# Kernel tuning notes

Hardware: AMD Instinct MI355X
Metric: run time of the kernel (lower is better)

The kernel has to match this reference:

```python
import jax, jax.numpy as jnp
import numpy as np

B, S, D_MODEL = 2, 2048, 4096
N_HEADS, N_KV, HEAD_DIM = 32, 8, 128
N_GROUPS = N_HEADS // N_KV
QKV_DIM = (N_HEADS + 2 * N_KV) * HEAD_DIM


def _rope_tables(seq_len, head_dim, base=10000.0):
    inv_freq = 1.0 / (base ** (np.arange(0, head_dim, 2, dtype=np.float32) / head_dim))
    t = np.arange(seq_len, dtype=np.float32)
    freqs = np.outer(t, inv_freq)                      # [S, D/2]
    emb = np.concatenate([freqs, freqs], axis=-1)      # [S, D]
    return jnp.asarray(np.cos(emb)), jnp.asarray(np.sin(emb))


def setup_inputs() -> dict:
    key = jax.random.key(0)
    k1, k2, k3 = jax.random.split(key, 3)
    cos, sin = _rope_tables(S, HEAD_DIM)
    return {
        "hidden_states": jax.random.normal(k1, (B, S, D_MODEL), dtype=jnp.float32),
        "cos": cos,
        "sin": sin,
        "W_qkv": jax.random.normal(k2, (D_MODEL, QKV_DIM), dtype=jnp.float32) * (D_MODEL ** -0.5),
        "W_out": jax.random.normal(k3, (D_MODEL, D_MODEL), dtype=jnp.float32) * (D_MODEL ** -0.5),
    }


def _rotate_half(x):
    x1, x2 = jnp.split(x, 2, axis=-1)
    return jnp.concatenate([-x2, x1], axis=-1)


def _apply_rope(x, cos, sin):
    # x: [b, h, s, d]; cos/sin: [s, d]
    c = cos[None, None, :, :]
    s = sin[None, None, :, :]
    return x * c + _rotate_half(x) * s


def reference(hidden_states, cos, sin, W_qkv, W_out):
    b, s, _ = hidden_states.shape
    qkv = jnp.einsum("bsm,mq->bsq", hidden_states, W_qkv)
    q_end = N_HEADS * HEAD_DIM
    kv_sz = N_KV * HEAD_DIM
    q = qkv[..., :q_end].reshape(b, s, N_HEADS, HEAD_DIM).transpose(0, 2, 1, 3)
    k = qkv[..., q_end:q_end + kv_sz].reshape(b, s, N_KV, HEAD_DIM).transpose(0, 2, 1, 3)
    v = qkv[..., q_end + kv_sz:].reshape(b, s, N_KV, HEAD_DIM).transpose(0, 2, 1, 3)

    q = _apply_rope(q, cos, sin)          # [b, H, s, d]
    k = _apply_rope(k, cos, sin)          # [b, KV, s, d] (equiv. to repeat->rope->stride slice)

    # GQA without materializing repeated KV: group query heads per KV head.
    qg = q.reshape(b, N_KV, N_GROUPS, s, HEAD_DIM)
    scale = HEAD_DIM ** -0.5
    scores = jnp.einsum("bkgqd,bkpd->bkgqp", qg, k) * scale  # [b, KV, G, s, s]
    causal = jnp.tril(jnp.ones((s, s), dtype=bool))
    scores = jnp.where(causal, scores, jnp.finfo(scores.dtype).min)
    probs = jax.nn.softmax(scores, axis=-1)
    out = jnp.einsum("bkgqp,bkpd->bkgqd", probs, v)           # [b, KV, G, s, d]
    out = out.reshape(b, N_HEADS, s, HEAD_DIM).transpose(0, 2, 1, 3).reshape(b, s, D_MODEL)
    return jnp.einsum("bsm,mn->bsn", out, W_out)
```

## Files before the change

### kernel.cpp

```cpp
#include <hip/hip_runtime.h>


typedef __bf16 bf16;
typedef bf16 bf16x8 __attribute__((ext_vector_type(8)));
typedef bf16 bf16x4 __attribute__((ext_vector_type(4)));
typedef float f32x4 __attribute__((ext_vector_type(4)));
typedef unsigned int u32;
typedef u32 u32x4 __attribute__((ext_vector_type(4)));

#define B_ 2
#define S_ 2048
#define DM 4096
#define NH 32
#define NKV 8
#define HD 128
#define QKV_DIM 6144

typedef __attribute__((address_space(3))) void lds_void;
typedef const __attribute__((address_space(1))) void glb_void;

__device__ __forceinline__ void gld_lds16(const bf16* g, bf16* l) {
  __builtin_amdgcn_global_load_lds((glb_void*)g, (lds_void*)l, 16, 0, 0);
}

__device__ __forceinline__ u32 bf16bits(float x) {
  union { bf16 h; unsigned short s; } u;
  u.h = (bf16)x;
  return (u32)u.s;
}

__global__ __launch_bounds__(256) void cast_f32_bf16(const float* __restrict__ src,
                                                     bf16* __restrict__ dst, int n) {
  int i = (blockIdx.x * 256 + threadIdx.x) * 4;
  float4 v = *(const float4*)(src + i);
  bf16x4 o;
  o[0] = (bf16)v.x; o[1] = (bf16)v.y; o[2] = (bf16)v.z; o[3] = (bf16)v.w;
  *(bf16x4*)(dst + i) = o;
}

__global__ __launch_bounds__(256) void transpose_cast_w(const float* __restrict__ W,
                                                        bf16* __restrict__ Wt,
                                                        int K, int N) {
  __shared__ float tile[64][65];
  const int n0 = blockIdx.x * 64, k0 = blockIdx.y * 64;
  const int t = threadIdx.x, j = t & 63, i0 = t >> 6;
  for (int p = 0; p < 16; ++p) {
    int i = i0 + p * 4;
    tile[i][j] = W[(size_t)(k0 + i) * N + n0 + j];
  }
  __syncthreads();
  for (int p = 0; p < 16; ++p) {
    int n = i0 + p * 4;
    Wt[(size_t)(n0 + n) * K + k0 + j] = (bf16)tile[j][n];
  }
}

__global__ __launch_bounds__(256) void transpose_v(const bf16* __restrict__ qkv,
                                                   bf16* __restrict__ v_t) {
  __shared__ bf16 tile[64][65];
  const int s0 = blockIdx.x * 64;
  const int d0 = blockIdx.y * 64;
  const int bk = blockIdx.z;
  const int b = bk >> 3, kv = bk & 7;
  const int t = threadIdx.x, j = t & 63, i0 = t >> 6;
  const bf16* src = qkv + (size_t)b * S_ * QKV_DIM + 5120 + kv * HD;
  for (int p = 0; p < 16; ++p) {
    int i = i0 + p * 4;
    tile[i][j] = src[(size_t)(s0 + i) * QKV_DIM + d0 + j];
  }
  __syncthreads();
  bf16* dst = v_t + ((size_t)bk * HD + d0) * S_ + s0;
  for (int p = 0; p < 16; ++p) {
    int dd = i0 + p * 4;
    dst[(size_t)dd * S_ + j] = tile[j][dd];
  }
}

__global__ __launch_bounds__(128) void rope_kernel(const bf16* __restrict__ qkv,
                                                   const float* __restrict__ cosT,
                                                   const float* __restrict__ sinT,
                                                   bf16* __restrict__ q_r,
                                                   bf16* __restrict__ k_r) {
  const int bs = blockIdx.x;
  const int b = bs >> 11, s = bs & 2047;
  const int d = threadIdx.x;
  const float cv = cosT[s * HD + d];
  const float sv = sinT[s * HD + d];
  const bf16* row = qkv + (size_t)bs * QKV_DIM;
  const float scale = 0.08838834764831845f;
  for (int h = 0; h < NH; ++h) {
    float x = (float)row[h * HD + d];
    float xr = (d < 64) ? -(float)row[h * HD + d + 64] : (float)row[h * HD + d - 64];
    q_r[(((size_t)(b * NH + h)) * S_ + s) * HD + d] = (bf16)((x * cv + xr * sv) * scale);
  }
  for (int kv = 0; kv < NKV; ++kv) {
    float x = (float)row[DM + kv * HD + d];
    float xr = (d < 64) ? -(float)row[DM + kv * HD + d + 64] : (float)row[DM + kv * HD + d - 64];
    k_r[(((size_t)(b * NKV + kv)) * S_ + s) * HD + d] = (bf16)(x * cv + xr * sv);
  }
}

#define BAR() __builtin_amdgcn_s_barrier()
#define LGKM0() asm volatile("s_waitcnt lgkmcnt(0)" ::: "memory")
#define VM6() asm volatile("s_waitcnt vmcnt(6)" ::: "memory")
#define VM0() asm volatile("s_waitcnt vmcnt(0)" ::: "memory")
#define VMNONE() do {} while (0)
#define PRIO1() __builtin_amdgcn_s_setprio(1)
#define PRIO0() __builtin_amdgcn_s_setprio(0)

#define MFMA16(MH)                                                                   \
  do {                                                                               \
    _Pragma("unroll") for (int mm = 0; mm < 4; ++mm) {                               \
      _Pragma("unroll") for (int nn = 0; nn < 4; ++nn) {                             \
        acc[(MH)*4 + mm][nn] = __builtin_amdgcn_mfma_f32_16x16x32_bf16(              \
            af[mm], bfr[nn], acc[(MH)*4 + mm][nn], 0, 0, 0);                         \
      }                                                                              \
    }                                                                                \
  } while (0)

#define TILE4(T, P, VMEND)                                                           \
  do {                                                                               \
    ldA(P, 0, 0); ldB(P, 0);                                                         \
    stage_idx(4 * (T) + 7);                                                          \
    BAR(); LGKM0();                                                                  \
    PRIO1(); MFMA16(0); PRIO0(); BAR();                                              \
    ldA(P, 0, 1);                                                                    \
    stage_idx(4 * (T) + 8);                                                          \
    BAR(); LGKM0();                                                                  \
    PRIO1(); MFMA16(1); PRIO0(); BAR();                                              \
    ldA(P, 1, 0); ldB(P, 1);                                                         \
    stage_idx(4 * (T) + 9);                                                          \
    BAR(); LGKM0();                                                                  \
    PRIO1(); MFMA16(0); PRIO0(); BAR();                                              \
    ldA(P, 1, 1);                                                                    \
    stage_idx(4 * (T) + 10);                                                         \
    BAR(); LGKM0();                                                                  \
    PRIO1(); MFMA16(1); PRIO0();                                                     \
    VMEND; BAR();                                                                    \
  } while (0)

template <bool OUT_BF16>
__global__ __launch_bounds__(512, 2) void gemm256_bt(const bf16* __restrict__ A,
                                                     const bf16* __restrict__ Bt,
                                                     void* __restrict__ Cout,
                                                     int M, int N, int K) {
  extern __shared__ char lds[];
  const int NT = K >> 6;

  const int nwg = gridDim.x;
  const int cpx = nwg >> 3;
  const int wg = (blockIdx.x & 7) * cpx + (blockIdx.x >> 3);
  const int nbx = N >> 8;
  const int bx = wg % nbx, by = wg / nbx;
  const int m0 = by * 256, n0 = bx * 256;

  const int t = threadIdx.x;
  const int w = t >> 6, lane = t & 63;
  const int wr = w >> 2, wc = w & 3;
  const int quad = lane >> 4, c = lane & 15;

  const int aOff = (((wr * 128 + c) * 64 + quad * 16) ^ ((c & 8) << 2));
  const int bOff = (((wc * 64 + c) * 64 + quad * 16) ^ ((c & 8) << 2)) + 32768;

  const int srow = w * 32 + (lane >> 2);
  const int scol = (((lane & 3) ^ ((lane >> 4) & 2)) << 3);
  const bf16* Abase = A + (size_t)(m0 + srow) * K + scol;
  const bf16* Bbase = Bt + (size_t)(n0 + srow) * K + scol;
  const size_t rs16 = (size_t)16 * K;

  auto stage_idx = [&](int H) {
    if (H >= 4 * NT) return;
    const int tS = H >> 2, jS = H & 3;
    const int kh = jS >> 1;
    const int kbase = tS * 64 + kh * 32;
    const int regionOff = ((tS & 1) << 16) + ((jS & 1) << 15) + (kh << 14) + (w << 11);
    const bf16* g = ((jS & 1) ? Bbase : Abase) + kbase;
    char* l = lds + regionOff;
    gld_lds16(g, (bf16*)l);
    gld_lds16(g + rs16, (bf16*)(l + 1024));
  };

  bf16x8 af[4], bfr[4];
  auto ldA = [&](int P, int s, int mh) {
    const char* base = lds + P * 65536 + s * 16384 + mh * 4096 + aOff;
    af[0] = *(const bf16x8*)(base);
    af[1] = *(const bf16x8*)(base + 1024);
    af[2] = *(const bf16x8*)(base + 2048);
    af[3] = *(const bf16x8*)(base + 3072);
  };
  auto ldB = [&](int P, int s) {
    const char* base = lds + P * 65536 + s * 16384 + bOff;
    bfr[0] = *(const bf16x8*)(base);
    bfr[1] = *(const bf16x8*)(base + 1024);
    bfr[2] = *(const bf16x8*)(base + 2048);
    bfr[3] = *(const bf16x8*)(base + 3072);
  };

  f32x4 acc[8][4];
#pragma unroll
  for (int i = 0; i < 8; ++i)
#pragma unroll
    for (int j = 0; j < 4; ++j) acc[i][j] = (f32x4){0.f, 0.f, 0.f, 0.f};

#pragma unroll
  for (int hh = 0; hh < 7; ++hh) stage_idx(hh);
  VM6();
  BAR();

  for (int tt = 0; tt < NT - 2; tt += 2) {
    TILE4(tt, 0, VM6());
    TILE4(tt + 1, 1, VM6());
  }
  TILE4(NT - 2, 0, VM0());
  TILE4(NT - 1, 1, VMNONE());

  const int crow = m0 + wr * 128 + quad * 4;
  const int ccol = n0 + wc * 64 + c;
#pragma unroll
  for (int mf = 0; mf < 8; ++mf)
#pragma unroll
    for (int nn = 0; nn < 4; ++nn) {
      const int row = crow + mf * 16;
      const int col = ccol + nn * 16;
      if constexpr (OUT_BF16) {
        bf16* Cp = (bf16*)Cout;
#pragma unroll
        for (int r = 0; r < 4; ++r) Cp[(size_t)(row + r) * N + col] = (bf16)acc[mf][nn][r];
      } else {
        float* Cp = (float*)Cout;
#pragma unroll
        for (int r = 0; r < 4; ++r) Cp[(size_t)(row + r) * N + col] = acc[mf][nn][r];
      }
    }
}

#define SKS 136
#define SVS 40
__global__ __launch_bounds__(256) void attn_kernel(const bf16* __restrict__ q_r,
                                                   const bf16* __restrict__ k_r,
                                                   const bf16* __restrict__ v_t,
                                                   bf16* __restrict__ attn_out) {
  __shared__ bf16 Ks[32 * SKS];
  __shared__ bf16 Vs[128 * SVS];

  const int bh = blockIdx.x;
  const int b = bh >> 5, h = bh & 31;
  const int kv = h >> 2;
  const int q0 = blockIdx.y * 64;
  const int t = threadIdx.x, w = t >> 6, lane = t & 63;
  const int quad = lane >> 4, c = lane & 15;
  const int myq = q0 + w * 16 + c;

  const bf16* qrow = q_r + ((size_t)(b * NH + h) * S_ + myq) * HD;
  bf16x8 qf[4];
#pragma unroll
  for (int kk = 0; kk < 4; ++kk) qf[kk] = *(const bf16x8*)(qrow + quad * 8 + kk * 32);

  float m_i = -1e30f, l_i = 0.f;
  f32x4 o_acc[8];
#pragma unroll
  for (int n = 0; n < 8; ++n) o_acc[n] = (f32x4){0.f, 0.f, 0.f, 0.f};

  const bf16* kb_ptr = k_r + (size_t)(b * NKV + kv) * S_ * HD;
  const bf16* vb_ptr = v_t + (size_t)(b * NKV + kv) * HD * S_;

  const int nch = (q0 + 64) >> 5;
  const int ks_key = t >> 3, ks_doff = (t & 7) * 16;
  const int vs_d = t >> 1, vs_koff = (t & 1) * 16;
  const int src0 = c + 32 * (quad & 1);
  const int src1 = src0 + 16;
  const bool hiTile = (quad & 2) != 0;

  for (int ch = 0; ch < nch; ++ch) {
    const int kb = ch * 32;
    __syncthreads();
    {
      const bf16* kp = kb_ptr + (size_t)(kb + ks_key) * HD + ks_doff;
      bf16x8 kv0 = *(const bf16x8*)(kp);
      bf16x8 kv1 = *(const bf16x8*)(kp + 8);
      const bf16* vp = vb_ptr + (size_t)vs_d * S_ + kb + vs_koff;
      bf16x8 vv0 = *(const bf16x8*)(vp);
      bf16x8 vv1 = *(const bf16x8*)(vp + 8);
      *(bf16x8*)(Ks + ks_key * SKS + ks_doff) = kv0;
      *(bf16x8*)(Ks + ks_key * SKS + ks_doff + 8) = kv1;
      *(bf16x8*)(Vs + vs_d * SVS + vs_koff) = vv0;
      *(bf16x8*)(Vs + vs_d * SVS + vs_koff + 8) = vv1;
    }
    __syncthreads();

    if (kb <= q0 + w * 16 + 15) {
      f32x4 st0 = (f32x4){0.f, 0.f, 0.f, 0.f};
      f32x4 st1 = (f32x4){0.f, 0.f, 0.f, 0.f};
#pragma unroll
      for (int kk = 0; kk < 4; ++kk) {
        bf16x8 kf0 = *(const bf16x8*)(Ks + c * SKS + quad * 8 + kk * 32);
        bf16x8 kf1 = *(const bf16x8*)(Ks + (16 + c) * SKS + quad * 8 + kk * 32);
        st0 = __builtin_amdgcn_mfma_f32_16x16x32_bf16(kf0, qf[kk], st0, 0, 0, 0);
        st1 = __builtin_amdgcn_mfma_f32_16x16x32_bf16(kf1, qf[kk], st1, 0, 0, 0);
      }

      float v0[4], v1[4];
      const bool needMask = (kb + 31 > q0 + w * 16);
#pragma unroll
      for (int r = 0; r < 4; ++r) { v0[r] = st0[r]; v1[r] = st1[r]; }
      if (needMask) {
        const int key0 = kb + quad * 4;
#pragma unroll
        for (int r = 0; r < 4; ++r) {
          if (key0 + r > myq) v0[r] = -1e30f;
          if (key0 + 16 + r > myq) v1[r] = -1e30f;
        }
      }

      float mloc = fmaxf(fmaxf(fmaxf(v0[0], v0[1]), fmaxf(v0[2], v0[3])),
                         fmaxf(fmaxf(v1[0], v1[1]), fmaxf(v1[2], v1[3])));
      mloc = fmaxf(mloc, __shfl_xor(mloc, 16, 64));
      mloc = fmaxf(mloc, __shfl_xor(mloc, 32, 64));
      const float mnew = fmaxf(m_i, mloc);
      float e0[4], e1[4];
      float sum = 0.f;
#pragma unroll
      for (int r = 0; r < 4; ++r) {
        e0[r] = __expf(v0[r] - mnew);
        e1[r] = __expf(v1[r] - mnew);
        sum += e0[r] + e1[r];
      }
      sum += __shfl_xor(sum, 16, 64);
      sum += __shfl_xor(sum, 32, 64);
      const float alpha = __expf(m_i - mnew);
      m_i = mnew;
      l_i = l_i * alpha + sum;

      u32 pk[4];
#pragma unroll
      for (int r = 0; r < 4; ++r) pk[r] = bf16bits(e0[r]) | (bf16bits(e1[r]) << 16);
      u32 a0[4], a1[4];
#pragma unroll
      for (int r = 0; r < 4; ++r) {
        a0[r] = (u32)__shfl((int)pk[r], src0, 64);
        a1[r] = (u32)__shfl((int)pk[r], src1, 64);
      }
      u32 w0, w1, w2, w3;
      if (hiTile) {
        w0 = (a0[0] >> 16) | (a0[1] & 0xffff0000u);
        w1 = (a0[2] >> 16) | (a0[3] & 0xffff0000u);
        w2 = (a1[0] >> 16) | (a1[1] & 0xffff0000u);
        w3 = (a1[2] >> 16) | (a1[3] & 0xffff0000u);
      } else {
        w0 = (a0[0] & 0xffffu) | (a0[1] << 16);
        w1 = (a0[2] & 0xffffu) | (a0[3] << 16);
        w2 = (a1[0] & 0xffffu) | (a1[1] << 16);
        w3 = (a1[2] & 0xffffu) | (a1[3] << 16);
      }
      bf16x8 pf = __builtin_bit_cast(bf16x8, (u32x4){w0, w1, w2, w3});

      float alpha_o[4];
#pragma unroll
      for (int r = 0; r < 4; ++r) alpha_o[r] = __shfl(alpha, quad * 4 + r, 64);

#pragma unroll
      for (int n = 0; n < 8; ++n) {
#pragma unroll
        for (int r = 0; r < 4; ++r) o_acc[n][r] *= alpha_o[r];
      }
#pragma unroll
      for (int n = 0; n < 8; ++n) {
        bf16x8 vf = *(const bf16x8*)(Vs + (n * 16 + c) * SVS + quad * 8);
        o_acc[n] = __builtin_amdgcn_mfma_f32_16x16x32_bf16(pf, vf, o_acc[n], 0, 0, 0);
      }
    }
  }

  float l_o[4];
#pragma unroll
  for (int r = 0; r < 4; ++r) l_o[r] = __shfl(l_i, quad * 4 + r, 64);
#pragma unroll
  for (int n = 0; n < 8; ++n)
#pragma unroll
    for (int r = 0; r < 4; ++r) {
      const int row = q0 + w * 16 + quad * 4 + r;
      const float ov = o_acc[n][r] / l_o[r];
      attn_out[((size_t)b * S_ + row) * DM + h * HD + n * 16 + c] = (bf16)ov;
    }
}

extern "C" void kernel_launch(void* const* d_in, const int* in_sizes, int n_in,
                              void* d_out, int out_size, void* d_ws, size_t ws_size,
                              hipStream_t stream) {
  const float* hidden = (const float*)d_in[0];
  const float* cosT = (const float*)d_in[1];
  const float* sinT = (const float*)d_in[2];
  const float* Wqkv = (const float*)d_in[3];
  const float* Wout = (const float*)d_in[4];
  float* out = (float*)d_out;
  char* ws = (char*)d_ws;

  bf16* WqkvT = (bf16*)(ws + 0);
  bf16* q_r = (bf16*)(ws + 0);
  bf16* k_r = (bf16*)(ws + 33554432);
  bf16* WoutT = (bf16*)(ws + 50331648);
  bf16* h_bf = (bf16*)(ws + 83886080);
  bf16* attn_out = (bf16*)(ws + 83886080);
  bf16* v_t = (bf16*)(ws + 117440512);
  bf16* qkv = (bf16*)d_out;

  static bool attr_set = false;
  if (!attr_set) {
    hipFuncSetAttribute(reinterpret_cast<const void*>(&gemm256_bt<true>),
                        hipFuncAttributeMaxDynamicSharedMemorySize, 131072);
    hipFuncSetAttribute(reinterpret_cast<const void*>(&gemm256_bt<false>),
                        hipFuncAttributeMaxDynamicSharedMemorySize, 131072);
    attr_set = true;
  }

  cast_f32_bf16<<<dim3(16384), dim3(256), 0, stream>>>(hidden, h_bf, B_ * S_ * DM);
  transpose_cast_w<<<dim3(QKV_DIM / 64, DM / 64), dim3(256), 0, stream>>>(Wqkv, WqkvT, DM, QKV_DIM);
  transpose_cast_w<<<dim3(DM / 64, DM / 64), dim3(256), 0, stream>>>(Wout, WoutT, DM, DM);
  gemm256_bt<true><<<dim3((QKV_DIM / 256) * ((B_ * S_) / 256)), dim3(512), 131072, stream>>>(
      h_bf, WqkvT, (void*)qkv, B_ * S_, QKV_DIM, DM);
  rope_kernel<<<dim3(B_ * S_), dim3(128), 0, stream>>>(qkv, cosT, sinT, q_r, k_r);
  transpose_v<<<dim3(S_ / 64, HD / 64, B_ * NKV), dim3(256), 0, stream>>>(qkv, v_t);
  attn_kernel<<<dim3(B_ * NH, S_ / 64), dim3(256), 0, stream>>>(q_r, k_r, v_t, attn_out);
  gemm256_bt<false><<<dim3((DM / 256) * ((B_ * S_) / 256)), dim3(512), 131072, stream>>>(
      attn_out, WoutT, (void*)out, B_ * S_, DM, DM);
}
```

Measured before the change: 807.2 us.

## Restructure GEMM main loop into two barriers per tile with split fragment registers

```diff
diff --git a/kernel.cpp b/kernel.cpp
--- a/kernel.cpp
+++ b/kernel.cpp
@@ -101,43 +101,41 @@
 }
 
 #define BAR() __builtin_amdgcn_s_barrier()
-#define LGKM0() asm volatile("s_waitcnt lgkmcnt(0)" ::: "memory")
-#define VM6() asm volatile("s_waitcnt vmcnt(6)" ::: "memory")
+#define VM4() asm volatile("s_waitcnt vmcnt(4)" ::: "memory")
 #define VM0() asm volatile("s_waitcnt vmcnt(0)" ::: "memory")
-#define VMNONE() do {} while (0)
 #define PRIO1() __builtin_amdgcn_s_setprio(1)
 #define PRIO0() __builtin_amdgcn_s_setprio(0)
 
-#define MFMA16(MH)                                                                   \
+#define MFMA16(AF, BF, MH)                                                           \
   do {                                                                               \
     _Pragma("unroll") for (int mm = 0; mm < 4; ++mm) {                               \
       _Pragma("unroll") for (int nn = 0; nn < 4; ++nn) {                             \
         acc[(MH)*4 + mm][nn] = __builtin_amdgcn_mfma_f32_16x16x32_bf16(              \
-            af[mm], bfr[nn], acc[(MH)*4 + mm][nn], 0, 0, 0);                         \
+            AF[mm], BF[nn], acc[(MH)*4 + mm][nn], 0, 0, 0);                          \
       }                                                                              \
     }                                                                                \
   } while (0)
 
-#define TILE4(T, P, VMEND)                                                           \
+#define GTILE(P, DO_S0, DO_S1, VMEND)                                                \
   do {                                                                               \
-    ldA(P, 0, 0); ldB(P, 0);                                                         \
-    stage_idx(4 * (T) + 7);                                                          \
-    BAR(); LGKM0();                                                                  \
-    PRIO1(); MFMA16(0); PRIO0(); BAR();                                              \
-    ldA(P, 0, 1);                                                                    \
-    stage_idx(4 * (T) + 8);                                                          \
-    BAR(); LGKM0();                                                                  \
-    PRIO1(); MFMA16(1); PRIO0(); BAR();                                              \
-    ldA(P, 1, 0); ldB(P, 1);                                                         \
-    stage_idx(4 * (T) + 9);                                                          \
-    BAR(); LGKM0();                                                                  \
-    PRIO1(); MFMA16(0); PRIO0(); BAR();                                              \
-    ldA(P, 1, 1);                                                                    \
-    stage_idx(4 * (T) + 10);                                                         \
-    BAR(); LGKM0();                                                                  \
-    PRIO1(); MFMA16(1); PRIO0();                                                     \
-    VMEND; BAR();                                                                    \
+    BAR();                                                                           \
+    ldAf(P, 0);                                           \
+    ldB0(P);                                                        \
+    if (DO_S0) { stageB(P ^ 1, 1, 96); stageA(P ^ 1, 1, 96); }                       \
+    ldAg(P, 0);                                           \
+    ldB1(P);                                                        \
+    PRIO1(); MFMA16(af, b0, 0); PRIO0();                                             \
+    ldAf(P, 1);                                   \
+    PRIO1(); MFMA16(ag, b0, 1); PRIO0();                                             \
+    ldAg(P, 1);                                                                      \
+    BAR();                                     \
+    if (DO_S1) { stageA(P, 0, 128); stageB(P, 0, 128); }                             \
+    PRIO1(); MFMA16(af, b1, 0); MFMA16(ag, b1, 1); PRIO0();                          \
+    VMEND;                                                                           \
   } while (0)
+
+#define ADV()                                                                        \
+  do { gA += 64; gA2 += 64; gB += 64; gB2 += 64; } while (0)
 
 template <bool OUT_BF16>
 __global__ __launch_bounds__(512, 2) void gemm256_bt(const bf16* __restrict__ A,
@@ -164,36 +162,51 @@
 
   const int srow = w * 32 + (lane >> 2);
   const int scol = (((lane & 3) ^ ((lane >> 4) & 2)) << 3);
-  const bf16* Abase = A + (size_t)(m0 + srow) * K + scol;
-  const bf16* Bbase = Bt + (size_t)(n0 + srow) * K + scol;
-  const size_t rs16 = (size_t)16 * K;
-
-  auto stage_idx = [&](int H) {
-    if (H >= 4 * NT) return;
-    const int tS = H >> 2, jS = H & 3;
-    const int kh = jS >> 1;
-    const int kbase = tS * 64 + kh * 32;
-    const int regionOff = ((tS & 1) << 16) + ((jS & 1) << 15) + (kh << 14) + (w << 11);
-    const bf16* g = ((jS & 1) ? Bbase : Abase) + kbase;
-    char* l = lds + regionOff;
-    gld_lds16(g, (bf16*)l);
-    gld_lds16(g + rs16, (bf16*)(l + 1024));
-  };
-
-  bf16x8 af[4], bfr[4];
-  auto ldA = [&](int P, int s, int mh) {
-    const char* base = lds + P * 65536 + s * 16384 + mh * 4096 + aOff;
+  const bf16* gA = A + (size_t)(m0 + srow) * K + scol;
+  const bf16* gA2 = gA + (size_t)16 * K;
+  const bf16* gB = Bt + (size_t)(n0 + srow) * K + scol;
+  const bf16* gB2 = gB + (size_t)16 * K;
+  char* ldsw = lds + (w << 11);
+
+  auto stageA = [&](int P, int kh, int ke) {
+    bf16* l = (bf16*)(ldsw + (P << 16) + (kh << 14));
+    gld_lds16(gA + ke, l);
+    gld_lds16(gA2 + ke, (bf16*)((char*)l + 1024));
+  };
+  auto stageB = [&](int P, int kh, int ke) {
+    bf16* l = (bf16*)(ldsw + (P << 16) + 32768 + (kh << 14));
+    gld_lds16(gB + ke, l);
+    gld_lds16(gB2 + ke, (bf16*)((char*)l + 1024));
+  };
+
+  bf16x8 af[4], ag[4], b0[4], b1[4];
+  auto ldAf = [&](int P, int kh) {
+    const char* base = lds + P * 65536 + kh * 16384 + aOff;
     af[0] = *(const bf16x8*)(base);
     af[1] = *(const bf16x8*)(base + 1024);
     af[2] = *(const bf16x8*)(base + 2048);
     af[3] = *(const bf16x8*)(base + 3072);
   };
-  auto ldB = [&](int P, int s) {
-    const char* base = lds + P * 65536 + s * 16384 + bOff;
-    bfr[0] = *(const bf16x8*)(base);
-    bfr[1] = *(const bf16x8*)(base + 1024);
-    bfr[2] = *(const bf16x8*)(base + 2048);
-    bfr[3] = *(const bf16x8*)(base + 3072);
+  auto ldAg = [&](int P, int kh) {
+    const char* base = lds + P * 65536 + kh * 16384 + 4096 + aOff;
+    ag[0] = *(const bf16x8*)(base);
+    ag[1] = *(const bf16x8*)(base + 1024);
+    ag[2] = *(const bf16x8*)(base + 2048);
+    ag[3] = *(const bf16x8*)(base + 3072);
+  };
+  auto ldB0 = [&](int P) {
+    const char* base = lds + P * 65536 + bOff;
+    b0[0] = *(const bf16x8*)(base);
+    b0[1] = *(const bf16x8*)(base + 1024);
+    b0[2] = *(const bf16x8*)(base + 2048);
+    b0[3] = *(const bf16x8*)(base + 3072);
+  };
+  auto ldB1 = [&](int P) {
+    const char* base = lds + P * 65536 + 16384 + bOff;
+    b1[0] = *(const bf16x8*)(base);
+    b1[1] = *(const bf16x8*)(base + 1024);
+    b1[2] = *(const bf16x8*)(base + 2048);
+    b1[3] = *(const bf16x8*)(base + 3072);
   };
 
   f32x4 acc[8][4];
@@ -202,17 +215,17 @@
 #pragma unroll
     for (int j = 0; j < 4; ++j) acc[i][j] = (f32x4){0.f, 0.f, 0.f, 0.f};
 
-#pragma unroll
-  for (int hh = 0; hh < 7; ++hh) stage_idx(hh);
-  VM6();
-  BAR();
+  stageA(0, 0, 0); stageB(0, 0, 0);
+  stageA(0, 1, 32); stageB(0, 1, 32);
+  stageA(1, 0, 64); stageB(1, 0, 64);
+  VM4();
 
   for (int tt = 0; tt < NT - 2; tt += 2) {
-    TILE4(tt, 0, VM6());
-    TILE4(tt + 1, 1, VM6());
-  }
-  TILE4(NT - 2, 0, VM0());
-  TILE4(NT - 1, 1, VMNONE());
+    GTILE(0, 1, 1, VM4()); ADV();
+    GTILE(1, 1, 1, VM4()); ADV();
+  }
+  GTILE(0, 1, 0, VM0());
+  GTILE(1, 0, 0, (void)0);
 
   const int crow = m0 + wr * 128 + quad * 4;
   const int ccol = n0 + wc * 64 + c;
```

After: 780.6 us. 1.03x faster.
